# Performance work log

Hardware: AMD Instinct MI355X
Metric: run time of the kernel (lower is better)

## Reference

```python
import jax, jax.numpy as jnp
import numpy as np

K = 1024      # num_embeddings
D = 256       # embedding_dim
BETA = 0.25


def setup_inputs() -> dict:
    key = jax.random.key(0)
    k1, k2 = jax.random.split(key)
    latents = jax.random.normal(k1, (32, D, 32, 32), dtype=jnp.float32)
    # nn.Embedding weight init: uniform(-1/K, 1/K)
    weight = jax.random.uniform(k2, (K, D), dtype=jnp.float32,
                                minval=-1.0 / K, maxval=1.0 / K)
    return {"latents": latents, "weight": weight}


def reference(latents, weight):
    # NCHW -> NHWC
    lat = jnp.transpose(latents, (0, 2, 3, 1))          # [B,H,W,D]
    lat_shape = lat.shape
    flat = lat.reshape(-1, D)                           # [N,D]

    dist = (jnp.sum(flat ** 2, axis=1, keepdims=True)
            - 2.0 * jnp.matmul(flat, weight.T)
            + jnp.sum(weight ** 2, axis=1))             # [N,K]

    min_ind = jnp.argmin(dist, axis=1)                  # [N]
    min_embed = jax.nn.one_hot(min_ind, K, dtype=flat.dtype)  # [N,K]

    # one-hot @ weight == direct gather
    z_q = jnp.take(weight, min_ind, axis=0).reshape(lat_shape)  # [B,H,W,D]

    sg = jax.lax.stop_gradient
    loss = (jnp.mean((sg(z_q) - lat) ** 2)
            + BETA * jnp.mean((z_q - sg(lat)) ** 2))

    # straight-through estimator
    z_q_st = lat + sg(z_q - lat)

    e_mean = jnp.mean(min_embed, axis=0)                # [K]
    perplexity = jnp.exp(-jnp.sum(e_mean * jnp.log(e_mean + 1e-10)))

    z_q_out = jnp.transpose(z_q_st, (0, 3, 1, 2))       # NHWC -> NCHW
    return (loss, z_q_out, perplexity, min_embed, min_ind[:, None])
```

## Files before the change

kernel.cpp:

```cpp
#include <hip/hip_runtime.h>

#define KN 1024
#define DD 256
#define NTOT 32768
#define HW 1024

#define OFF_LOSS 0
#define OFF_ZQ   1
#define OFF_PERP 8388609
#define OFF_EMB  8388610
#define OFF_IND  41943042

#define WS_WSUM2_OFF 4112
#define WS_WBH_OFF   8208
#define WS_WBL_OFF   (8208 + 524288)

#define XS_STRIDE 260
#define THR 3.0e-4f

typedef __bf16 bf16x8 __attribute__((ext_vector_type(8)));
typedef float  f32x4  __attribute__((ext_vector_type(4)));
typedef unsigned short ushort_t;

#define SM_XS    0
#define SM_XFH   33280
#define SM_XFL   49664
#define SM_WSC   66048
#define SM_PART  70144
#define SM_REDV  70144
#define SM_ROWM  70656
#define SM_CCNT  70784
#define SM_CLIST 70912
#define SM_FV    71936
#define SM_ASUM  72960
#define SM_BI    73088
#define SM_LRED  73216
#define SM_SIZE  73248

__device__ __forceinline__ unsigned short bf16_rne(float f) {
    unsigned u = __float_as_uint(f);
    return (unsigned short)((u + 0x7FFFu + ((u >> 16) & 1u)) >> 16);
}

__device__ __forceinline__ float exact_dist(const float* xs, const float* wsC,
                                            const float* asum,
                                            const float* __restrict__ w,
                                            int r, int k) {
    float a = 0.f;
    const float4* wr = (const float4*)(w + k * DD);
    const float4* xr = (const float4*)(xs + r * XS_STRIDE);
    #pragma unroll 4
    for (int q = 0; q < 64; ++q) {
        const float4 wv = wr[q];
        const float4 xv = xr[q];
        a = fmaf(xv.x, wv.x, a);
        a = fmaf(xv.y, wv.y, a);
        a = fmaf(xv.z, wv.z, a);
        a = fmaf(xv.w, wv.w, a);
    }
    return (asum[r] - 2.0f * a) + wsC[k];
}

__global__ __launch_bounds__(256) void vq_prep(const float* __restrict__ w,
                                               float* __restrict__ wsum2,
                                               ushort_t* __restrict__ wBh,
                                               ushort_t* __restrict__ wBl) {
    const int k = blockIdx.x;
    const int d = threadIdx.x;
    float v = w[k * DD + d];
    {
        const int c = k >> 4, s0 = d >> 5, g = (d >> 3) & 3, j = d & 7;
        const int lane = (k & 15) | (g << 4);
        const int idx = (((c * 8 + s0) * 64 + lane) << 3) + j;
        const unsigned short hh = bf16_rne(v);
        wBh[idx] = hh;
        wBl[idx] = bf16_rne(v - __uint_as_float((unsigned)hh << 16));
    }
    float s = v * v;
    #pragma unroll
    for (int off = 32; off; off >>= 1) s += __shfl_down(s, off, 64);
    __shared__ float wsum[4];
    const int wave = d >> 6, lane = d & 63;
    if (lane == 0) wsum[wave] = s;
    __syncthreads();
    if (d == 0) wsum2[k] = (wsum[0] + wsum[1]) + (wsum[2] + wsum[3]);
}

__global__ __launch_bounds__(256, 2) void vq_main(const float* __restrict__ lat,
                                                  const float* __restrict__ w,
                                                  const float* __restrict__ wsum2,
                                                  const ushort_t* __restrict__ wBh,
                                                  const ushort_t* __restrict__ wBl,
                                                  float* __restrict__ out,
                                                  unsigned* __restrict__ cnt,
                                                  double* __restrict__ lossSum) {
    extern __shared__ char smem[];
    float*    xs    = (float*)(smem + SM_XS);
    ushort_t* xfH   = (ushort_t*)(smem + SM_XFH);
    ushort_t* xfL   = (ushort_t*)(smem + SM_XFL);
    float*    wsC   = (float*)(smem + SM_WSC);
    float*    part  = (float*)(smem + SM_PART);
    float*    redv  = (float*)(smem + SM_REDV);
    float*    rowm  = (float*)(smem + SM_ROWM);
    unsigned* ccnt  = (unsigned*)(smem + SM_CCNT);
    int*      clist = (int*)(smem + SM_CLIST);
    float*    fv    = (float*)(smem + SM_FV);
    float*    asum  = (float*)(smem + SM_ASUM);
    int*      bi    = (int*)(smem + SM_BI);
    double*   lred  = (double*)(smem + SM_LRED);

    const int n0  = blockIdx.x * 32;
    const int b   = n0 >> 10;
    const int hw0 = n0 & 1023;
    const int tid = threadIdx.x;
    const int l   = tid & 63;
    const int wv  = tid >> 6;

    {
        const float* base = lat + (size_t)b * (DD * HW) + hw0;
        const int rr = tid & 31, dl = tid >> 5;
        #pragma unroll
        for (int it = 0; it < 32; ++it) {
            const int d = it * 8 + dl;
            xs[rr * XS_STRIDE + d] = base[d * HW + rr];
        }
        for (int i = tid; i < KN; i += 256) wsC[i] = wsum2[i];
    }
    __syncthreads();

    #pragma unroll
    for (int h = 0; h < 2; ++h) {
        const int r = tid & 15, seg = tid >> 4;
        float p = 0.f;
        #pragma unroll
        for (int i = 0; i < 16; ++i) {
            float x = xs[(h * 16 + r) * XS_STRIDE + seg * 16 + i];
            p += x * x;
        }
        part[seg * 17 + r] = p;
        __syncthreads();
        if (tid < 16) {
            float a = 0.f;
            #pragma unroll
            for (int s = 0; s < 16; ++s) a += part[s * 17 + tid];
            asum[h * 16 + tid] = a;
        }
        __syncthreads();
    }

    #pragma unroll
    for (int i = 0; i < 4; ++i) {
        const int u  = tid + i * 256;
        const int rt = u >> 9, s0 = (u >> 6) & 7, ll = u & 63;
        const int row = rt * 16 + (ll & 15);
        const int d0  = s0 * 32 + (ll >> 4) * 8;
        const float4 x0 = *(const float4*)(xs + row * XS_STRIDE + d0);
        const float4 x1 = *(const float4*)(xs + row * XS_STRIDE + d0 + 4);
        float xv[8] = {x0.x, x0.y, x0.z, x0.w, x1.x, x1.y, x1.z, x1.w};
        unsigned hh[8], lo[8];
        #pragma unroll
        for (int j = 0; j < 8; ++j) {
            hh[j] = bf16_rne(xv[j]);
            lo[j] = bf16_rne(xv[j] - __uint_as_float(hh[j] << 16));
        }
        uint4 ph, pl;
        ph.x = hh[0] | (hh[1] << 16); ph.y = hh[2] | (hh[3] << 16);
        ph.z = hh[4] | (hh[5] << 16); ph.w = hh[6] | (hh[7] << 16);
        pl.x = lo[0] | (lo[1] << 16); pl.y = lo[2] | (lo[3] << 16);
        pl.z = lo[4] | (lo[5] << 16); pl.w = lo[6] | (lo[7] << 16);
        *(uint4*)(xfH + u * 8) = ph;
        *(uint4*)(xfL + u * 8) = pl;
    }
    __syncthreads();

    f32x4 acc[2][16];
    #pragma unroll
    for (int rt = 0; rt < 2; ++rt)
        #pragma unroll
        for (int c = 0; c < 16; ++c)
            acc[rt][c] = (f32x4){0.f, 0.f, 0.f, 0.f};

    for (int s0 = 0; s0 < 8; ++s0) {
        const bf16x8 ah0 = *(const bf16x8*)(xfH + ((0 * 8 + s0) * 64 + l) * 8);
        const bf16x8 ah1 = *(const bf16x8*)(xfH + ((1 * 8 + s0) * 64 + l) * 8);
        const bf16x8 al0 = *(const bf16x8*)(xfL + ((0 * 8 + s0) * 64 + l) * 8);
        const bf16x8 al1 = *(const bf16x8*)(xfL + ((1 * 8 + s0) * 64 + l) * 8);
        #pragma unroll
        for (int c = 0; c < 16; ++c) {
            const size_t boff = ((size_t)(((wv * 16 + c) * 8 + s0) * 64 + l)) * 8;
            const bf16x8 bh = *(const bf16x8*)(wBh + boff);
            const bf16x8 bl = *(const bf16x8*)(wBl + boff);
            acc[0][c] = __builtin_amdgcn_mfma_f32_16x16x32_bf16(ah0, bh, acc[0][c], 0, 0, 0);
            acc[1][c] = __builtin_amdgcn_mfma_f32_16x16x32_bf16(ah1, bh, acc[1][c], 0, 0, 0);
            acc[0][c] = __builtin_amdgcn_mfma_f32_16x16x32_bf16(ah0, bl, acc[0][c], 0, 0, 0);
            acc[1][c] = __builtin_amdgcn_mfma_f32_16x16x32_bf16(ah1, bl, acc[1][c], 0, 0, 0);
            acc[0][c] = __builtin_amdgcn_mfma_f32_16x16x32_bf16(al0, bh, acc[0][c], 0, 0, 0);
            acc[1][c] = __builtin_amdgcn_mfma_f32_16x16x32_bf16(al1, bh, acc[1][c], 0, 0, 0);
        }
    }

    float rmv[2][4];
    #pragma unroll
    for (int rt = 0; rt < 2; ++rt)
        #pragma unroll
        for (int q = 0; q < 4; ++q) rmv[rt][q] = 3.4e38f;
    #pragma unroll
    for (int c = 0; c < 16; ++c) {
        const float cv = wsC[(wv * 16 + c) * 16 + (l & 15)];
        #pragma unroll
        for (int rt = 0; rt < 2; ++rt) {
            #pragma unroll
            for (int q = 0; q < 4; ++q) {
                const float dv = fmaf(-2.0f, acc[rt][c][q], cv);
                acc[rt][c][q] = dv;
                rmv[rt][q] = fminf(rmv[rt][q], dv);
            }
        }
    }
    #pragma unroll
    for (int rt = 0; rt < 2; ++rt)
        #pragma unroll
        for (int q = 0; q < 4; ++q) {
            float m = rmv[rt][q];
            #pragma unroll
            for (int off = 1; off < 16; off <<= 1) m = fminf(m, __shfl_xor(m, off, 64));
            rmv[rt][q] = m;
        }
    if ((l & 15) == 0) {
        const int g = l >> 4;
        #pragma unroll
        for (int rt = 0; rt < 2; ++rt)
            #pragma unroll
            for (int q = 0; q < 4; ++q)
                redv[wv * 32 + rt * 16 + g * 4 + q] = rmv[rt][q];
    }
    __syncthreads();
    if (tid < 32) {
        float m = redv[tid];
        #pragma unroll
        for (int ww = 1; ww < 4; ++ww) m = fminf(m, redv[ww * 32 + tid]);
        rowm[tid] = m;
        ccnt[tid] = 0u;
    }
    __syncthreads();

    #pragma unroll
    for (int rt = 0; rt < 2; ++rt) {
        #pragma unroll
        for (int q = 0; q < 4; ++q) {
            const int row = rt * 16 + ((l >> 4) << 2) + q;
            const float lim = rowm[row] + THR;
            #pragma unroll
            for (int c = 0; c < 16; ++c) {
                if (acc[rt][c][q] <= lim) {
                    const unsigned pos = atomicAdd(&ccnt[row], 1u);
                    if (pos < 8) clist[row * 8 + pos] = (wv * 16 + c) * 16 + (l & 15);
                }
            }
        }
    }
    __syncthreads();

    {
        const int r = tid >> 3, ci = tid & 7;
        const unsigned cc = ccnt[r];
        if (cc >= 2u) {
            if (cc <= 8u) {
                if ((unsigned)ci < cc)
                    fv[r * 8 + ci] = exact_dist(xs, wsC, asum, w, r, clist[r * 8 + ci]);
            } else if (ci == 0) {
                float bvv = 3.4e38f; int bkk = 0;
                for (int k = 0; k < KN; ++k) {
                    const float dvv = exact_dist(xs, wsC, asum, w, r, k);
                    if (dvv < bvv) { bvv = dvv; bkk = k; }
                }
                bi[r] = bkk;
            }
        }
    }
    __syncthreads();
    if (tid < 32) {
        const unsigned cc = ccnt[tid];
        int kk;
        if (cc == 1u) kk = clist[tid * 8];
        else if (cc <= 8u) {
            float v = fv[tid * 8]; kk = clist[tid * 8];
            for (unsigned ci = 1; ci < cc; ++ci) {
                const float ov = fv[tid * 8 + ci];
                const int   ok = clist[tid * 8 + ci];
                if (ov < v || (ov == v && ok < kk)) { v = ov; kk = ok; }
            }
        } else kk = bi[tid];
        bi[tid] = kk;
        out[OFF_IND + n0 + tid] = (float)kk;
        atomicAdd(&cnt[kk], 1u);
    }
    __syncthreads();

    {
        float2* emb2 = reinterpret_cast<float2*>(out + OFF_EMB) + (size_t)n0 * (KN / 2);
        #pragma unroll
        for (int it = 0; it < 64; ++it) {
            const int f = it * 256 + tid;
            const int r = f >> 9;
            const int kq = (f & 511) * 2;
            const int tt = bi[r];
            float2 v2;
            v2.x = (kq     == tt) ? 1.0f : 0.0f;
            v2.y = (kq + 1 == tt) ? 1.0f : 0.0f;
            emb2[f] = v2;
        }
    }

    #pragma unroll
    for (int h = 0; h < 2; ++h) {
        const int n0h = n0 + h * 16;
        const int bb = n0h >> 10, hw0h = n0h & 1023;
        float* zq_out = out + OFF_ZQ + (size_t)bb * (DD * HW) + hw0h;
        const int jj = tid & 15, db = tid >> 4;
        const int krow = bi[h * 16 + jj];
        float lsum = 0.f;
        #pragma unroll
        for (int it = 0; it < 16; ++it) {
            const int d = it * 16 + db;
            const float latv = xs[(h * 16 + jj) * XS_STRIDE + d];
            const float zq   = w[krow * DD + d];
            const float dif  = zq - latv;
            zq_out[d * HW + jj] = latv + dif;
            lsum = fmaf(dif, dif, lsum);
        }
        float s2 = lsum;
        #pragma unroll
        for (int off = 32; off; off >>= 1) s2 += __shfl_down(s2, off, 64);
        if ((tid & 63) == 0) lred[wv] = (double)s2;
        __syncthreads();
        if (tid == 0) {
            double t = (lred[0] + lred[1]) + (lred[2] + lred[3]);
            atomicAdd(lossSum, t);
        }
        __syncthreads();
    }
}

__global__ __launch_bounds__(1024) void vq_finalize(const unsigned* __restrict__ cnt,
                                                    const double* __restrict__ lossSum,
                                                    float* __restrict__ out) {
    const int t = threadIdx.x;
    __shared__ float red[16];
    const float e = (float)cnt[t] * (1.0f / 32768.0f);
    float s = e * logf(e + 1e-10f);
    #pragma unroll
    for (int off = 32; off; off >>= 1) s += __shfl_down(s, off, 64);
    const int wave = t >> 6, lane = t & 63;
    if (lane == 0) red[wave] = s;
    __syncthreads();
    if (t == 0) {
        float tot = 0.f;
        #pragma unroll
        for (int i = 0; i < 16; ++i) tot += red[i];
        out[OFF_PERP] = expf(-tot);
        const float m = (float)(lossSum[0] * (1.0 / 8388608.0));
        out[OFF_LOSS] = m + 0.25f * m;
    }
}

extern "C" void kernel_launch(void* const* d_in, const int* in_sizes, int n_in,
                              void* d_out, int out_size, void* d_ws, size_t ws_size,
                              hipStream_t stream) {
    const float* lat = (const float*)d_in[0];
    const float* w   = (const float*)d_in[1];

    char* ws = (char*)d_ws;
    double*   lossSum = (double*)ws;
    unsigned* cnt     = (unsigned*)(ws + 8);
    float*    wsum2   = (float*)(ws + WS_WSUM2_OFF);
    ushort_t* wBh     = (ushort_t*)(ws + WS_WBH_OFF);
    ushort_t* wBl     = (ushort_t*)(ws + WS_WBL_OFF);
    float*    out     = (float*)d_out;

    hipMemsetAsync(d_ws, 0, 4104, stream);

    hipFuncSetAttribute(reinterpret_cast<const void*>(vq_main),
                        hipFuncAttributeMaxDynamicSharedMemorySize, SM_SIZE);

    vq_prep<<<KN, 256, 0, stream>>>(w, wsum2, wBh, wBl);
    vq_main<<<NTOT / 32, 256, SM_SIZE, stream>>>(lat, w, wsum2, wBh, wBl, out, cnt, lossSum);
    vq_finalize<<<1, 1024, 0, stream>>>(cnt, lossSum, out);
}
```

Before: 147.8 us.

## Split codebook columns across eight waves and prefetch weight fragments

Doubles the block to 512 threads so each of eight waves handles 128 codebook entries instead of 256. This halves the per-wave accumulator registers and MFMA chain. It also adds a two-deep register prefetch of the bf16 hi/lo weight fragments, overlapping global loads with MFMA work. The trade-off is more waves per block, larger reduction arrays, and extra idle threads in the epilogue and loss phases, which remain restricted to 256 threads.

```diff
diff --git a/kernel.cpp b/kernel.cpp
--- a/kernel.cpp
+++ b/kernel.cpp
@@ -28,14 +28,14 @@
 #define SM_WSC   66048
 #define SM_PART  70144
 #define SM_REDV  70144
-#define SM_ROWM  70656
-#define SM_CCNT  70784
-#define SM_CLIST 70912
-#define SM_FV    71936
-#define SM_ASUM  72960
-#define SM_BI    73088
-#define SM_LRED  73216
-#define SM_SIZE  73248
+#define SM_ROWM  71168
+#define SM_CCNT  71296
+#define SM_CLIST 71424
+#define SM_FV    72448
+#define SM_ASUM  73472
+#define SM_BI    73600
+#define SM_LRED  73728
+#define SM_SIZE  73760
 
 __device__ __forceinline__ unsigned short bf16_rne(float f) {
     unsigned u = __float_as_uint(f);
@@ -86,7 +86,7 @@
     if (d == 0) wsum2[k] = (wsum[0] + wsum[1]) + (wsum[2] + wsum[3]);
 }
 
-__global__ __launch_bounds__(256, 2) void vq_main(const float* __restrict__ lat,
+__global__ __launch_bounds__(512, 2) void vq_main(const float* __restrict__ lat,
                                                   const float* __restrict__ w,
                                                   const float* __restrict__ wsum2,
                                                   const ushort_t* __restrict__ wBh,
@@ -120,24 +120,26 @@
         const float* base = lat + (size_t)b * (DD * HW) + hw0;
         const int rr = tid & 31, dl = tid >> 5;
         #pragma unroll
-        for (int it = 0; it < 32; ++it) {
-            const int d = it * 8 + dl;
+        for (int it = 0; it < 16; ++it) {
+            const int d = it * 16 + dl;
             xs[rr * XS_STRIDE + d] = base[d * HW + rr];
         }
-        for (int i = tid; i < KN; i += 256) wsC[i] = wsum2[i];
+        for (int i = tid; i < KN; i += 512) wsC[i] = wsum2[i];
     }
     __syncthreads();
 
     #pragma unroll
     for (int h = 0; h < 2; ++h) {
-        const int r = tid & 15, seg = tid >> 4;
-        float p = 0.f;
-        #pragma unroll
-        for (int i = 0; i < 16; ++i) {
-            float x = xs[(h * 16 + r) * XS_STRIDE + seg * 16 + i];
-            p += x * x;
-        }
-        part[seg * 17 + r] = p;
+        if (tid < 256) {
+            const int r = tid & 15, seg = tid >> 4;
+            float p = 0.f;
+            #pragma unroll
+            for (int i = 0; i < 16; ++i) {
+                float x = xs[(h * 16 + r) * XS_STRIDE + seg * 16 + i];
+                p += x * x;
+            }
+            part[seg * 17 + r] = p;
+        }
         __syncthreads();
         if (tid < 16) {
             float a = 0.f;
@@ -149,8 +151,8 @@
     }
 
     #pragma unroll
-    for (int i = 0; i < 4; ++i) {
-        const int u  = tid + i * 256;
+    for (int i = 0; i < 2; ++i) {
+        const int u  = tid + i * 512;
         const int rt = u >> 9, s0 = (u >> 6) & 7, ll = u & 63;
         const int row = rt * 16 + (ll & 15);
         const int d0  = s0 * 32 + (ll >> 4) * 8;
@@ -173,23 +175,44 @@
     }
     __syncthreads();
 
-    f32x4 acc[2][16];
+    f32x4 acc[2][8];
     #pragma unroll
     for (int rt = 0; rt < 2; ++rt)
         #pragma unroll
-        for (int c = 0; c < 16; ++c)
+        for (int c = 0; c < 8; ++c)
             acc[rt][c] = (f32x4){0.f, 0.f, 0.f, 0.f};
 
-    for (int s0 = 0; s0 < 8; ++s0) {
-        const bf16x8 ah0 = *(const bf16x8*)(xfH + ((0 * 8 + s0) * 64 + l) * 8);
-        const bf16x8 ah1 = *(const bf16x8*)(xfH + ((1 * 8 + s0) * 64 + l) * 8);
-        const bf16x8 al0 = *(const bf16x8*)(xfL + ((0 * 8 + s0) * 64 + l) * 8);
-        const bf16x8 al1 = *(const bf16x8*)(xfL + ((1 * 8 + s0) * 64 + l) * 8);
-        #pragma unroll
-        for (int c = 0; c < 16; ++c) {
-            const size_t boff = ((size_t)(((wv * 16 + c) * 8 + s0) * 64 + l)) * 8;
-            const bf16x8 bh = *(const bf16x8*)(wBh + boff);
-            const bf16x8 bl = *(const bf16x8*)(wBl + boff);
+    {
+        bf16x8 ah0, ah1, al0, al1;
+        bf16x8 pbh0, pbl0, pbh1, pbl1;
+
+        #define BOFF(s0_, c_) (((size_t)(((wv * 8 + (c_)) * 8 + (s0_)) * 64 + l)) * 8)
+        pbh0 = *(const bf16x8*)(wBh + BOFF(0, 0));
+        pbl0 = *(const bf16x8*)(wBl + BOFF(0, 0));
+        pbh1 = *(const bf16x8*)(wBh + BOFF(0, 1));
+        pbl1 = *(const bf16x8*)(wBl + BOFF(0, 1));
+
+        #pragma unroll
+        for (int it = 0; it < 64; ++it) {
+            const int s0 = it >> 3, c = it & 7;
+            if (c == 0) {
+                ah0 = *(const bf16x8*)(xfH + ((0 * 8 + s0) * 64 + l) * 8);
+                ah1 = *(const bf16x8*)(xfH + ((1 * 8 + s0) * 64 + l) * 8);
+                al0 = *(const bf16x8*)(xfL + ((0 * 8 + s0) * 64 + l) * 8);
+                al1 = *(const bf16x8*)(xfL + ((1 * 8 + s0) * 64 + l) * 8);
+            }
+            bf16x8 bh, bl;
+            if ((it & 1) == 0) { bh = pbh0; bl = pbl0; } else { bh = pbh1; bl = pbl1; }
+            if (it + 2 < 64) {
+                const int nit = it + 2, ns = nit >> 3, nc = nit & 7;
+                if ((it & 1) == 0) {
+                    pbh0 = *(const bf16x8*)(wBh + BOFF(ns, nc));
+                    pbl0 = *(const bf16x8*)(wBl + BOFF(ns, nc));
+                } else {
+                    pbh1 = *(const bf16x8*)(wBh + BOFF(ns, nc));
+                    pbl1 = *(const bf16x8*)(wBl + BOFF(ns, nc));
+                }
+            }
             acc[0][c] = __builtin_amdgcn_mfma_f32_16x16x32_bf16(ah0, bh, acc[0][c], 0, 0, 0);
             acc[1][c] = __builtin_amdgcn_mfma_f32_16x16x32_bf16(ah1, bh, acc[1][c], 0, 0, 0);
             acc[0][c] = __builtin_amdgcn_mfma_f32_16x16x32_bf16(ah0, bl, acc[0][c], 0, 0, 0);
@@ -197,6 +220,7 @@
             acc[0][c] = __builtin_amdgcn_mfma_f32_16x16x32_bf16(al0, bh, acc[0][c], 0, 0, 0);
             acc[1][c] = __builtin_amdgcn_mfma_f32_16x16x32_bf16(al1, bh, acc[1][c], 0, 0, 0);
         }
+        #undef BOFF
     }
 
     float rmv[2][4];
@@ -205,8 +229,8 @@
         #pragma unroll
         for (int q = 0; q < 4; ++q) rmv[rt][q] = 3.4e38f;
     #pragma unroll
-    for (int c = 0; c < 16; ++c) {
-        const float cv = wsC[(wv * 16 + c) * 16 + (l & 15)];
+    for (int c = 0; c < 8; ++c) {
+        const float cv = wsC[(wv * 8 + c) * 16 + (l & 15)];
         #pragma unroll
         for (int rt = 0; rt < 2; ++rt) {
             #pragma unroll
@@ -238,7 +262,7 @@
     if (tid < 32) {
         float m = redv[tid];
         #pragma unroll
-        for (int ww = 1; ww < 4; ++ww) m = fminf(m, redv[ww * 32 + tid]);
+        for (int ww = 1; ww < 8; ++ww) m = fminf(m, redv[ww * 32 + tid]);
         rowm[tid] = m;
         ccnt[tid] = 0u;
     }
@@ -251,17 +275,17 @@
             const int row = rt * 16 + ((l >> 4) << 2) + q;
             const float lim = rowm[row] + THR;
             #pragma unroll
-            for (int c = 0; c < 16; ++c) {
+            for (int c = 0; c < 8; ++c) {
                 if (acc[rt][c][q] <= lim) {
                     const unsigned pos = atomicAdd(&ccnt[row], 1u);
-                    if (pos < 8) clist[row * 8 + pos] = (wv * 16 + c) * 16 + (l & 15);
+                    if (pos < 8) clist[row * 8 + pos] = (wv * 8 + c) * 16 + (l & 15);
                 }
             }
         }
     }
     __syncthreads();
 
-    {
+    if (tid < 256) {
         const int r = tid >> 3, ci = tid & 7;
         const unsigned cc = ccnt[r];
         if (cc >= 2u) {
@@ -300,8 +324,8 @@
     {
         float2* emb2 = reinterpret_cast<float2*>(out + OFF_EMB) + (size_t)n0 * (KN / 2);
         #pragma unroll
-        for (int it = 0; it < 64; ++it) {
-            const int f = it * 256 + tid;
+        for (int it = 0; it < 32; ++it) {
+            const int f = it * 512 + tid;
             const int r = f >> 9;
             const int kq = (f & 511) * 2;
             const int tt = bi[r];
@@ -314,25 +338,27 @@
 
     #pragma unroll
     for (int h = 0; h < 2; ++h) {
-        const int n0h = n0 + h * 16;
-        const int bb = n0h >> 10, hw0h = n0h & 1023;
-        float* zq_out = out + OFF_ZQ + (size_t)bb * (DD * HW) + hw0h;
-        const int jj = tid & 15, db = tid >> 4;
-        const int krow = bi[h * 16 + jj];
-        float lsum = 0.f;
-        #pragma unroll
-        for (int it = 0; it < 16; ++it) {
-            const int d = it * 16 + db;
-            const float latv = xs[(h * 16 + jj) * XS_STRIDE + d];
-            const float zq   = w[krow * DD + d];
-            const float dif  = zq - latv;
-            zq_out[d * HW + jj] = latv + dif;
-            lsum = fmaf(dif, dif, lsum);
-        }
-        float s2 = lsum;
-        #pragma unroll
-        for (int off = 32; off; off >>= 1) s2 += __shfl_down(s2, off, 64);
-        if ((tid & 63) == 0) lred[wv] = (double)s2;
+        if (tid < 256) {
+            const int n0h = n0 + h * 16;
+            const int bb = n0h >> 10, hw0h = n0h & 1023;
+            float* zq_out = out + OFF_ZQ + (size_t)bb * (DD * HW) + hw0h;
+            const int jj = tid & 15, db = tid >> 4;
+            const int krow = bi[h * 16 + jj];
+            float lsum = 0.f;
+            #pragma unroll
+            for (int it = 0; it < 16; ++it) {
+                const int d = it * 16 + db;
+                const float latv = xs[(h * 16 + jj) * XS_STRIDE + d];
+                const float zq   = w[krow * DD + d];
+                const float dif  = zq - latv;
+                zq_out[d * HW + jj] = latv + dif;
+                lsum = fmaf(dif, dif, lsum);
+            }
+            float s2 = lsum;
+            #pragma unroll
+            for (int off = 32; off; off >>= 1) s2 += __shfl_down(s2, off, 64);
+            if ((tid & 63) == 0) lred[wv] = (double)s2;
+        }
         __syncthreads();
         if (tid == 0) {
             double t = (lred[0] + lred[1]) + (lred[2] + lred[3]);
@@ -384,6 +410,6 @@
                         hipFuncAttributeMaxDynamicSharedMemorySize, SM_SIZE);
 
     vq_prep<<<KN, 256, 0, stream>>>(w, wsum2, wBh, wBl);
-    vq_main<<<NTOT / 32, 256, SM_SIZE, stream>>>(lat, w, wsum2, wBh, wBl, out, cnt, lossSum);
+    vq_main<<<NTOT / 32, 512, SM_SIZE, stream>>>(lat, w, wsum2, wBh, wBl, out, cnt, lossSum);
     vq_finalize<<<1, 1024, 0, stream>>>(cnt, lossSum, out);
 }
```

New measurement: 131.0 us. -11.4%, faster.
